# Kernel tuning notes

Measured on AMD Instinct MI355X. Metric: run time of the kernel, lower is better.

Reference implementation:

```python
import jax, jax.numpy as jnp
import numpy as np


def setup_inputs() -> dict:
    key = jax.random.key(0)
    ks = jax.random.split(key, 7)
    B, Nc, Nt = 4, 2048, 2048
    D = 512          # key_size == representation_size
    H, E = 8, 64     # num_heads, head_dim = D // H
    return {
        "keys": jax.random.normal(ks[0], (B, Nc, D), dtype=jnp.float32),
        "values": jax.random.normal(ks[1], (B, Nc, D), dtype=jnp.float32),
        "query": jax.random.normal(ks[2], (B, Nt, D), dtype=jnp.float32),
        "Wk": jax.random.normal(ks[3], (H, D, E), dtype=jnp.float32) * 0.02,
        "Wv": jax.random.normal(ks[4], (H, D, E), dtype=jnp.float32) * 0.02,
        "Wq": jax.random.normal(ks[5], (H, D, E), dtype=jnp.float32) * 0.02,
        "Wout": jax.random.normal(ks[6], (D, D), dtype=jnp.float32) * 0.02,
    }


def reference(keys, values, query, Wk, Wv, Wq, Wout):
    # Batched per-head projections (replaces the per-head Python loop)
    k = jnp.einsum("bnd,hde->bhne", keys, Wk)    # [B,H,Nc,E]
    v = jnp.einsum("bnd,hde->bhne", values, Wv)  # [B,H,Nc,E]
    q = jnp.einsum("bnd,hde->bhne", query, Wq)   # [B,H,Nt,E]
    head_dim = q.shape[-1]
    # NOTE: original scales by head_dim (query.size()[2]), not sqrt(head_dim)
    scores = jnp.einsum("bhqe,bhke->bhqk", q, k) / head_dim
    attn = jax.nn.softmax(scores, axis=-1)
    out = jnp.einsum("bhqk,bhke->bhqe", attn, v)  # [B,H,Nt,E]
    # concat over heads (head-major feature order, matches torch.cat(dim=-1))
    B, H, Nt, E = out.shape
    out = jnp.transpose(out, (0, 2, 1, 3)).reshape(B, Nt, H * E)
    # final Linear (no bias): x @ Wout^T
    return out @ Wout.T
```

## Files before the change

### kernel.cpp

```cpp
#include <hip/hip_runtime.h>

#define B_   4
#define H_   8
#define NSEQ 2048
#define D_   512
#define E_   64

typedef __bf16 bf16x8 __attribute__((ext_vector_type(8)));
typedef float  f32x4  __attribute__((ext_vector_type(4)));

__device__ __forceinline__ unsigned short f2b(float f) {
    __bf16 h = (__bf16)f;
    return __builtin_bit_cast(unsigned short, h);
}
__device__ __forceinline__ bf16x8 ld_frag(const unsigned short* p) {
    return *reinterpret_cast<const bf16x8*>(p);
}
__device__ __forceinline__ void wave_lds_fence() {
    __asm__ __volatile__("s_waitcnt lgkmcnt(0)" ::: "memory");
}
__device__ __forceinline__ void async_copy16(const void* g, const unsigned short* l) {
    __builtin_amdgcn_global_load_lds(
        (const __attribute__((address_space(1))) unsigned int*)g,
        (__attribute__((address_space(3))) unsigned int*)l, 16, 0, 0);
}

__global__ __launch_bounds__(256)
void cast_w_kernel(const float* __restrict__ Wk, const float* __restrict__ Wv,
                   const float* __restrict__ Wq, const float* __restrict__ Wo,
                   unsigned short* __restrict__ okt, unsigned short* __restrict__ ovt,
                   unsigned short* __restrict__ oqt, unsigned short* __restrict__ oo) {
    int idx = blockIdx.x * 256 + threadIdx.x;
    int y = blockIdx.y;
    if (y == 3) { oo[idx] = f2b(Wo[idx]); return; }
    const float* src = y == 0 ? Wk : (y == 1 ? Wv : Wq);
    unsigned short* dst = y == 0 ? okt : (y == 1 ? ovt : oqt);
    float scl = (y == 2) ? 0.015625f : 1.0f;
    int hh = idx >> 15, rem = idx & 32767, d = rem >> 6, e = rem & 63;
    dst[hh * 32768 + e * 512 + d] = f2b(src[idx] * scl);
}

__global__ __launch_bounds__(256)
void xcast_kernel(const float* __restrict__ q, const float* __restrict__ k,
                  const float* __restrict__ v,
                  unsigned short* __restrict__ qx, unsigned short* __restrict__ kx,
                  unsigned short* __restrict__ vx) {
    const int y = blockIdx.y;
    const float* src = y == 0 ? q : (y == 1 ? k : v);
    unsigned short* dst = y == 0 ? qx : (y == 1 ? kx : vx);
    #pragma unroll
    for (int i = 0; i < 4; ++i) {
        int e = blockIdx.x * 4096 + i * 1024 + threadIdx.x * 4;
        float4 f = *reinterpret_cast<const float4*>(src + e);
        *reinterpret_cast<ushort4*>(dst + e) =
            make_ushort4(f2b(f.x), f2b(f.y), f2b(f.z), f2b(f.w));
    }
}

__global__ __launch_bounds__(256, 3)
void proj_gemm(const unsigned short* __restrict__ qx,
               const unsigned short* __restrict__ kx,
               const unsigned short* __restrict__ vx,
               const unsigned short* __restrict__ wqt,
               const unsigned short* __restrict__ wkt,
               const unsigned short* __restrict__ wvt,
               unsigned short* __restrict__ qb, unsigned short* __restrict__ kb,
               unsigned short* __restrict__ vtb) {
    const int m0  = blockIdx.x * 128;
    const int no0 = blockIdx.y * 64;
    const int which = blockIdx.z;
    const int tid = threadIdx.x;
    const int wave = tid >> 6, lane = tid & 63;
    const int quad = lane >> 4, l16 = lane & 15;

    const unsigned short* X = which == 0 ? qx : (which == 1 ? kx : vx);
    const unsigned short* W = which == 0 ? wqt : (which == 1 ? wkt : wvt);

    __shared__ unsigned short Ab[2][8192];
    __shared__ unsigned short Bb[2][4096];

    const unsigned short* Xp = X + (size_t)m0 * D_;
    const unsigned short* Wp = W + (size_t)no0 * D_;

    const int swzF = (l16 & 7) << 4;
    const int r8   = lane >> 3;
    const int sg   = lane & 7;
    const int colK = (sg * 16) ^ ((r8 & 7) << 4);

    #define PROJ_STAGE(kt, buf)                                                \
        {   _Pragma("unroll")                                                  \
            for (int i = 0; i < 4; ++i)                                        \
                async_copy16(                                                  \
                    (const char*)(Xp + (size_t)(wave * 32 + i * 8 + r8) * D_ + \
                                  (kt) * 64) + colK,                           \
                    &Ab[buf][(wave * 32 + i * 8) * 64]);                       \
            _Pragma("unroll")                                                  \
            for (int i = 0; i < 2; ++i)                                        \
                async_copy16(                                                  \
                    (const char*)(Wp + (size_t)(wave * 16 + i * 8 + r8) * D_ + \
                                  (kt) * 64) + colK,                           \
                    &Bb[buf][(wave * 16 + i * 8) * 64]);                       \
        }

    PROJ_STAGE(0, 0)
    __syncthreads();

    const f32x4 z = {0.f, 0.f, 0.f, 0.f};
    f32x4 acc[2][4];
    #pragma unroll
    for (int i = 0; i < 2; ++i)
        #pragma unroll
        for (int j = 0; j < 4; ++j) acc[i][j] = z;

    for (int kt = 0; kt < 8; ++kt) {
        const int cur = kt & 1;
        if (kt + 1 < 8) PROJ_STAGE(kt + 1, 1 - cur)
        #pragma unroll
        for (int kk = 0; kk < 2; ++kk) {
            const int co = ((kk * 64 + quad * 16) ^ swzF) >> 1;
            bf16x8 bfr[4];
            #pragma unroll
            for (int nt = 0; nt < 4; ++nt)
                bfr[nt] = ld_frag(&Bb[cur][(nt * 16 + l16) * 64 + co]);
            #pragma unroll
            for (int mt = 0; mt < 2; ++mt) {
                bf16x8 af = ld_frag(&Ab[cur][(wave * 32 + mt * 16 + l16) * 64 + co]);
                #pragma unroll
                for (int nt = 0; nt < 4; ++nt)
                    acc[mt][nt] = __builtin_amdgcn_mfma_f32_16x16x32_bf16(
                        af, bfr[nt], acc[mt][nt], 0, 0, 0);
            }
        }
        __syncthreads();
    }

    if (which != 2) {
        unsigned short (*Os)[72] = reinterpret_cast<unsigned short(*)[72]>(&Ab[0][0]);
        #pragma unroll
        for (int mt = 0; mt < 2; ++mt)
            #pragma unroll
            for (int nt = 0; nt < 4; ++nt)
                #pragma unroll
                for (int r = 0; r < 4; ++r)
                    Os[wave * 32 + mt * 16 + quad * 4 + r][nt * 16 + l16] =
                        f2b(acc[mt][nt][r]);
        __syncthreads();
        unsigned short* Y = (which == 0 ? qb : kb);
        #pragma unroll
        for (int i = 0; i < 4; ++i) {
            int idx = tid + i * 256;
            int row = idx >> 3, seg = idx & 7;
            *reinterpret_cast<uint4*>(Y + (size_t)(m0 + row) * D_ + no0 + seg * 8) =
                *reinterpret_cast<const uint4*>(&Os[row][seg * 8]);
        }
    } else {
        unsigned short (*Ot)[136] = reinterpret_cast<unsigned short(*)[136]>(&Ab[0][0]);
        #pragma unroll
        for (int mt = 0; mt < 2; ++mt)
            #pragma unroll
            for (int nt = 0; nt < 4; ++nt) {
                ushort4 o = make_ushort4(f2b(acc[mt][nt][0]), f2b(acc[mt][nt][1]),
                                         f2b(acc[mt][nt][2]), f2b(acc[mt][nt][3]));
                *reinterpret_cast<ushort4*>(
                    &Ot[nt * 16 + l16][wave * 32 + mt * 16 + quad * 4]) = o;
            }
        __syncthreads();
        const int b = m0 >> 11, nloc = m0 & 2047;
        #pragma unroll
        for (int i = 0; i < 4; ++i) {
            int idx = tid + i * 256;
            int lhe = idx >> 4, seg = idx & 15;
            int ghe = no0 + lhe;
            *reinterpret_cast<uint4*>(
                vtb + ((size_t)(b * H_ + (ghe >> 6)) * E_ + (ghe & 63)) * NSEQ +
                nloc + seg * 8) =
                *reinterpret_cast<const uint4*>(&Ot[lhe][seg * 8]);
        }
    }
    #undef PROJ_STAGE
}

__global__ __launch_bounds__(256, 4)
void attn_kernel(const unsigned short* __restrict__ qbp,
                 const unsigned short* __restrict__ kbp,
                 const unsigned short* __restrict__ vtbp,
                 unsigned short* __restrict__ aob) {
    const int L = blockIdx.x;
    const int bh = L & 31, qt = L >> 5;
    const int b = bh >> 3, h = bh & 7;
    const int n0 = qt * 64;
    const int tid = threadIdx.x;
    const int wave = tid >> 6, lane = tid & 63;
    const int quad = lane >> 4, l16 = lane & 15;

    __shared__ unsigned short Ks[2][4096];
    __shared__ unsigned short Vs[2][4096];
    __shared__ unsigned short Ps[4096];

    const unsigned short* kbase = kbp + (size_t)(b * NSEQ) * D_ + h * 64;
    const unsigned short* vbase = vtbp + (size_t)(b * H_ + h) * E_ * NSEQ;

    const int swzF = (l16 & 7) << 4;
    const int r8   = lane >> 3;
    const int sg   = lane & 7;
    const int colK = (sg * 16) ^ ((r8 & 7) << 4);

    bf16x8 qf[2];
    #pragma unroll
    for (int kk = 0; kk < 2; ++kk)
        qf[kk] = ld_frag(
            qbp + (size_t)(b * NSEQ + n0 + wave * 16 + l16) * D_ +
            h * 64 + kk * 32 + quad * 8);

    #define ATTN_STAGE(j, buf)                                                 \
        {   _Pragma("unroll")                                                  \
            for (int i = 0; i < 2; ++i) {                                      \
                async_copy16(                                                  \
                    (const char*)(kbase +                                      \
                        (size_t)((j) * 64 + wave * 16 + i * 8 + r8) * D_) + colK, \
                    &Ks[buf][wave * 1024 + i * 512]);                          \
                async_copy16(                                                  \
                    (const char*)(vbase +                                      \
                        (size_t)(wave * 16 + i * 8 + r8) * NSEQ + (j) * 64) + colK, \
                    &Vs[buf][wave * 1024 + i * 512]);                          \
            } }

    ATTN_STAGE(0, 0)
    __syncthreads();

    const f32x4 z = {0.f, 0.f, 0.f, 0.f};
    f32x4 oacc[4] = {z, z, z, z};
    float lacc = 0.f;

    for (int j = 0; j < NSEQ / 64; ++j) {
        const int cur = j & 1;
        if (j + 1 < NSEQ / 64) ATTN_STAGE(j + 1, 1 - cur)

        f32x4 sacc[4] = {z, z, z, z};
        #pragma unroll
        for (int kk = 0; kk < 2; ++kk)
            #pragma unroll
            for (int mg = 0; mg < 4; ++mg) {
                bf16x8 af = ld_frag(&Ks[cur][(mg * 16 + l16) * 64 +
                                             ((((kk * 64 + quad * 16) ^ swzF)) >> 1)]);
                sacc[mg] = __builtin_amdgcn_mfma_f32_16x16x32_bf16(
                    af, qf[kk], sacc[mg], 0, 0, 0);
            }

        {
            float ls = 0.f;
            #pragma unroll
            for (int mg = 0; mg < 4; ++mg) {
                float p0 = __expf(sacc[mg][0]);
                float p1 = __expf(sacc[mg][1]);
                float p2 = __expf(sacc[mg][2]);
                float p3 = __expf(sacc[mg][3]);
                ls += (p0 + p1) + (p2 + p3);
                ushort4 pk = make_ushort4(f2b(p0), f2b(p1), f2b(p2), f2b(p3));
                *reinterpret_cast<ushort4*>(
                    &Ps[(wave * 16 + l16) * 64 +
                        ((((mg * 32 + quad * 8) ^ swzF)) >> 1)]) = pk;
            }
            lacc += ls;
        }
        wave_lds_fence();

        #pragma unroll
        for (int kkv = 0; kkv < 2; ++kkv) {
            bf16x8 pf = ld_frag(&Ps[(wave * 16 + l16) * 64 +
                                    ((((kkv * 64 + quad * 16) ^ swzF)) >> 1)]);
            #pragma unroll
            for (int eg = 0; eg < 4; ++eg) {
                bf16x8 af = ld_frag(&Vs[cur][(eg * 16 + l16) * 64 +
                                             ((((kkv * 64 + quad * 16) ^ swzF)) >> 1)]);
                oacc[eg] = __builtin_amdgcn_mfma_f32_16x16x32_bf16(
                    af, pf, oacc[eg], 0, 0, 0);
            }
        }

        __syncthreads();
    }

    {
        float s = lacc;
        s += __shfl_xor(s, 16);
        s += __shfl_xor(s, 32);
        float li = 1.0f / s;
        unsigned short* op =
            aob + (size_t)(b * NSEQ + n0 + wave * 16 + l16) * D_ + h * 64 + quad * 4;
        #pragma unroll
        for (int eg = 0; eg < 4; ++eg) {
            ushort4 o = make_ushort4(f2b(oacc[eg][0] * li), f2b(oacc[eg][1] * li),
                                     f2b(oacc[eg][2] * li), f2b(oacc[eg][3] * li));
            *reinterpret_cast<ushort4*>(op + eg * 16) = o;
        }
    }
    #undef ATTN_STAGE
}

__global__ __launch_bounds__(256, 3)
void out_gemm(const unsigned short* __restrict__ A,
              const unsigned short* __restrict__ Wo,
              float* __restrict__ Out) {
    const int m0  = blockIdx.x * 128;
    const int no0 = blockIdx.y * 64;
    const int tid = threadIdx.x;
    const int wave = tid >> 6, lane = tid & 63;
    const int quad = lane >> 4, l16 = lane & 15;

    __shared__ unsigned short Ab[2][8192];
    __shared__ unsigned short Bb[2][4096];

    const unsigned short* Ap = A + (size_t)m0 * D_;
    const unsigned short* Bp = Wo + (size_t)no0 * D_;

    const int swzF = (l16 & 7) << 4;
    const int r8   = lane >> 3;
    const int sg   = lane & 7;
    const int colK = (sg * 16) ^ ((r8 & 7) << 4);

    #define OUT_STAGE(kt, buf)                                                 \
        {   _Pragma("unroll")                                                  \
            for (int i = 0; i < 4; ++i)                                        \
                async_copy16(                                                  \
                    (const char*)(Ap + (size_t)(wave * 32 + i * 8 + r8) * D_ + \
                                  (kt) * 64) + colK,                           \
                    &Ab[buf][(wave * 32 + i * 8) * 64]);                       \
            _Pragma("unroll")                                                  \
            for (int i = 0; i < 2; ++i)                                        \
                async_copy16(                                                  \
                    (const char*)(Bp + (size_t)(wave * 16 + i * 8 + r8) * D_ + \
                                  (kt) * 64) + colK,                           \
                    &Bb[buf][(wave * 16 + i * 8) * 64]);                       \
        }

    OUT_STAGE(0, 0)
    __syncthreads();

    const f32x4 z = {0.f, 0.f, 0.f, 0.f};
    f32x4 acc[2][4];
    #pragma unroll
    for (int i = 0; i < 2; ++i)
        #pragma unroll
        for (int j = 0; j < 4; ++j) acc[i][j] = z;

    for (int kt = 0; kt < 8; ++kt) {
        const int cur = kt & 1;
        if (kt + 1 < 8) OUT_STAGE(kt + 1, 1 - cur)
        #pragma unroll
        for (int kk = 0; kk < 2; ++kk) {
            const int co = ((kk * 64 + quad * 16) ^ swzF) >> 1;
            bf16x8 bfr[4];
            #pragma unroll
            for (int nt = 0; nt < 4; ++nt)
                bfr[nt] = ld_frag(&Bb[cur][(nt * 16 + l16) * 64 + co]);
            #pragma unroll
            for (int mt = 0; mt < 2; ++mt) {
                bf16x8 af = ld_frag(&Ab[cur][(wave * 32 + mt * 16 + l16) * 64 + co]);
                #pragma unroll
                for (int nt = 0; nt < 4; ++nt)
                    acc[mt][nt] = __builtin_amdgcn_mfma_f32_16x16x32_bf16(
                        af, bfr[nt], acc[mt][nt], 0, 0, 0);
            }
        }
        __syncthreads();
    }
    #pragma unroll
    for (int mt = 0; mt < 2; ++mt)
        #pragma unroll
        for (int nt = 0; nt < 4; ++nt)
            #pragma unroll
            for (int r = 0; r < 4; ++r)
                Out[(size_t)(m0 + wave * 32 + mt * 16 + quad * 4 + r) * D_ +
                    no0 + nt * 16 + l16] = acc[mt][nt][r];
    #undef OUT_STAGE
}

extern "C" void kernel_launch(void* const* d_in, const int* in_sizes, int n_in,
                              void* d_out, int out_size, void* d_ws, size_t ws_size,
                              hipStream_t stream) {
    const float* keys   = (const float*)d_in[0];
    const float* values = (const float*)d_in[1];
    const float* query  = (const float*)d_in[2];
    const float* Wk     = (const float*)d_in[3];
    const float* Wv     = (const float*)d_in[4];
    const float* Wq     = (const float*)d_in[5];
    const float* Wout   = (const float*)d_in[6];
    float* out = (float*)d_out;

    unsigned short* ws16 = (unsigned short*)d_ws;
    const size_t XN = (size_t)B_ * NSEQ * D_;
    const size_t WN = (size_t)H_ * D_ * E_;
    unsigned short* wkt = ws16;
    unsigned short* wvt = wkt + WN;
    unsigned short* wqt = wvt + WN;
    unsigned short* wob = wqt + WN;
    unsigned short* qb  = wob + WN;
    unsigned short* kb  = qb + XN;
    unsigned short* vtb = kb + XN;
    unsigned short* aob = vtb + XN;
    unsigned short* qx  = aob + XN;
    unsigned short* kx  = qx + XN;
    unsigned short* vx  = aob;

    cast_w_kernel<<<dim3(1024, 4), 256, 0, stream>>>(Wk, Wv, Wq, Wout,
                                                     wkt, wvt, wqt, wob);

    xcast_kernel<<<dim3(1024, 3), 256, 0, stream>>>(query, keys, values,
                                                    qx, kx, vx);

    proj_gemm<<<dim3(64, 8, 3), 256, 0, stream>>>(
        qx, kx, vx, wqt, wkt, wvt, qb, kb, vtb);

    attn_kernel<<<dim3(1024), 256, 0, stream>>>(qb, kb, vtb, aob);

    out_gemm<<<dim3(64, 8), 256, 0, stream>>>(aob, wob, out);
}
```

Before: 190.3 us.

## Use two waves per attention block, each handling 32 query rows

The attention kernel now runs 128 threads (2 waves) per block instead of 4 waves. Each wave processes two 16-row query groups, so every K and V fragment read from LDS feeds two MFMAs. This halves LDS fragment traffic per MFMA. The cost is more accumulator registers per wave, fewer waves per block to hide latency, and more async-copy work per thread.

```diff
diff --git a/kernel.cpp b/kernel.cpp
--- a/kernel.cpp
+++ b/kernel.cpp
@@ -180,7 +180,7 @@
     #undef PROJ_STAGE
 }
 
-__global__ __launch_bounds__(256, 4)
+__global__ __launch_bounds__(128, 2)
 void attn_kernel(const unsigned short* __restrict__ qbp,
                  const unsigned short* __restrict__ kbp,
                  const unsigned short* __restrict__ vtbp,
@@ -205,93 +205,113 @@
     const int sg   = lane & 7;
     const int colK = (sg * 16) ^ ((r8 & 7) << 4);
 
-    bf16x8 qf[2];
-    #pragma unroll
-    for (int kk = 0; kk < 2; ++kk)
-        qf[kk] = ld_frag(
-            qbp + (size_t)(b * NSEQ + n0 + wave * 16 + l16) * D_ +
-            h * 64 + kk * 32 + quad * 8);
+    bf16x8 qf[2][2];
+    #pragma unroll
+    for (int qg = 0; qg < 2; ++qg)
+        #pragma unroll
+        for (int kk = 0; kk < 2; ++kk)
+            qf[qg][kk] = ld_frag(
+                qbp + (size_t)(b * NSEQ + n0 + wave * 32 + qg * 16 + l16) * D_ +
+                h * 64 + kk * 32 + quad * 8);
 
     #define ATTN_STAGE(j, buf)                                                 \
         {   _Pragma("unroll")                                                  \
-            for (int i = 0; i < 2; ++i) {                                      \
+            for (int i = 0; i < 4; ++i) {                                      \
                 async_copy16(                                                  \
                     (const char*)(kbase +                                      \
-                        (size_t)((j) * 64 + wave * 16 + i * 8 + r8) * D_) + colK, \
-                    &Ks[buf][wave * 1024 + i * 512]);                          \
+                        (size_t)((j) * 64 + wave * 32 + i * 8 + r8) * D_) + colK, \
+                    &Ks[buf][(wave * 32 + i * 8) * 64]);                       \
                 async_copy16(                                                  \
                     (const char*)(vbase +                                      \
-                        (size_t)(wave * 16 + i * 8 + r8) * NSEQ + (j) * 64) + colK, \
-                    &Vs[buf][wave * 1024 + i * 512]);                          \
+                        (size_t)(wave * 32 + i * 8 + r8) * NSEQ + (j) * 64) + colK, \
+                    &Vs[buf][(wave * 32 + i * 8) * 64]);                       \
             } }
 
     ATTN_STAGE(0, 0)
     __syncthreads();
 
     const f32x4 z = {0.f, 0.f, 0.f, 0.f};
-    f32x4 oacc[4] = {z, z, z, z};
-    float lacc = 0.f;
+    f32x4 oacc[2][4];
+    #pragma unroll
+    for (int qg = 0; qg < 2; ++qg)
+        #pragma unroll
+        for (int eg = 0; eg < 4; ++eg) oacc[qg][eg] = z;
+    float lacc[2] = {0.f, 0.f};
 
     for (int j = 0; j < NSEQ / 64; ++j) {
         const int cur = j & 1;
         if (j + 1 < NSEQ / 64) ATTN_STAGE(j + 1, 1 - cur)
 
-        f32x4 sacc[4] = {z, z, z, z};
-        #pragma unroll
-        for (int kk = 0; kk < 2; ++kk)
+        f32x4 sacc[2][4];
+        #pragma unroll
+        for (int qg = 0; qg < 2; ++qg)
+            #pragma unroll
+            for (int mg = 0; mg < 4; ++mg) sacc[qg][mg] = z;
+        #pragma unroll
+        for (int kk = 0; kk < 2; ++kk) {
+            const int co = ((kk * 64 + quad * 16) ^ swzF) >> 1;
             #pragma unroll
             for (int mg = 0; mg < 4; ++mg) {
-                bf16x8 af = ld_frag(&Ks[cur][(mg * 16 + l16) * 64 +
-                                             ((((kk * 64 + quad * 16) ^ swzF)) >> 1)]);
-                sacc[mg] = __builtin_amdgcn_mfma_f32_16x16x32_bf16(
-                    af, qf[kk], sacc[mg], 0, 0, 0);
-            }
-
-        {
+                bf16x8 af = ld_frag(&Ks[cur][(mg * 16 + l16) * 64 + co]);
+                sacc[0][mg] = __builtin_amdgcn_mfma_f32_16x16x32_bf16(
+                    af, qf[0][kk], sacc[0][mg], 0, 0, 0);
+                sacc[1][mg] = __builtin_amdgcn_mfma_f32_16x16x32_bf16(
+                    af, qf[1][kk], sacc[1][mg], 0, 0, 0);
+            }
+        }
+
+        #pragma unroll
+        for (int qg = 0; qg < 2; ++qg) {
             float ls = 0.f;
+            const int prow = (wave * 32 + qg * 16 + l16) * 64;
             #pragma unroll
             for (int mg = 0; mg < 4; ++mg) {
-                float p0 = __expf(sacc[mg][0]);
-                float p1 = __expf(sacc[mg][1]);
-                float p2 = __expf(sacc[mg][2]);
-                float p3 = __expf(sacc[mg][3]);
+                float p0 = __expf(sacc[qg][mg][0]);
+                float p1 = __expf(sacc[qg][mg][1]);
+                float p2 = __expf(sacc[qg][mg][2]);
+                float p3 = __expf(sacc[qg][mg][3]);
                 ls += (p0 + p1) + (p2 + p3);
                 ushort4 pk = make_ushort4(f2b(p0), f2b(p1), f2b(p2), f2b(p3));
                 *reinterpret_cast<ushort4*>(
-                    &Ps[(wave * 16 + l16) * 64 +
-                        ((((mg * 32 + quad * 8) ^ swzF)) >> 1)]) = pk;
-            }
-            lacc += ls;
+                    &Ps[prow + ((((mg * 32 + quad * 8) ^ swzF)) >> 1)]) = pk;
+            }
+            lacc[qg] += ls;
         }
         wave_lds_fence();
 
         #pragma unroll
         for (int kkv = 0; kkv < 2; ++kkv) {
-            bf16x8 pf = ld_frag(&Ps[(wave * 16 + l16) * 64 +
-                                    ((((kkv * 64 + quad * 16) ^ swzF)) >> 1)]);
+            const int co = ((kkv * 64 + quad * 16) ^ swzF) >> 1;
+            bf16x8 pf0 = ld_frag(&Ps[(wave * 32 + l16) * 64 + co]);
+            bf16x8 pf1 = ld_frag(&Ps[(wave * 32 + 16 + l16) * 64 + co]);
             #pragma unroll
             for (int eg = 0; eg < 4; ++eg) {
-                bf16x8 af = ld_frag(&Vs[cur][(eg * 16 + l16) * 64 +
-                                             ((((kkv * 64 + quad * 16) ^ swzF)) >> 1)]);
-                oacc[eg] = __builtin_amdgcn_mfma_f32_16x16x32_bf16(
-                    af, pf, oacc[eg], 0, 0, 0);
+                bf16x8 af = ld_frag(&Vs[cur][(eg * 16 + l16) * 64 + co]);
+                oacc[0][eg] = __builtin_amdgcn_mfma_f32_16x16x32_bf16(
+                    af, pf0, oacc[0][eg], 0, 0, 0);
+                oacc[1][eg] = __builtin_amdgcn_mfma_f32_16x16x32_bf16(
+                    af, pf1, oacc[1][eg], 0, 0, 0);
             }
         }
 
         __syncthreads();
     }
 
-    {
-        float s = lacc;
+    #pragma unroll
+    for (int qg = 0; qg < 2; ++qg) {
+        float s = lacc[qg];
         s += __shfl_xor(s, 16);
         s += __shfl_xor(s, 32);
         float li = 1.0f / s;
         unsigned short* op =
-            aob + (size_t)(b * NSEQ + n0 + wave * 16 + l16) * D_ + h * 64 + quad * 4;
+            aob + (size_t)(b * NSEQ + n0 + wave * 32 + qg * 16 + l16) * D_ +
+            h * 64 + quad * 4;
         #pragma unroll
         for (int eg = 0; eg < 4; ++eg) {
-            ushort4 o = make_ushort4(f2b(oacc[eg][0] * li), f2b(oacc[eg][1] * li),
-                                     f2b(oacc[eg][2] * li), f2b(oacc[eg][3] * li));
+            ushort4 o = make_ushort4(f2b(oacc[qg][eg][0] * li),
+                                     f2b(oacc[qg][eg][1] * li),
+                                     f2b(oacc[qg][eg][2] * li),
+                                     f2b(oacc[qg][eg][3] * li));
             *reinterpret_cast<ushort4*>(op + eg * 16) = o;
         }
     }
@@ -412,7 +432,7 @@
     proj_gemm<<<dim3(64, 8, 3), 256, 0, stream>>>(
         qx, kx, vx, wqt, wkt, wvt, qb, kb, vtb);
 
-    attn_kernel<<<dim3(1024), 256, 0, stream>>>(qb, kb, vtb, aob);
+    attn_kernel<<<dim3(1024), 128, 0, stream>>>(qb, kb, vtb, aob);
 
     out_gemm<<<dim3(64, 8), 256, 0, stream>>>(aob, wob, out);
 }
```

Measured after the change: 196.1 us. 3.1% more time.

## Use 32x32 MFMA in attention with register-resident P and split-K waves

Applied to the files above, without the earlier changes.

Restructures the attention kernel to use 32x32x16 bf16 MFMA tiles. Each wave computes a 32-query by 32-key score block, and waves are split across the key halves. The probability tile is kept in registers via v_permlane32_swap instead of being staged through LDS, which removes the Ps buffer and its store/fence/reload. Partial outputs from the two key-half waves are reduced through LDS at the end. This adds an epilogue reduction, more accumulator registers and lower occupancy (launch bounds 4→3).

```diff
diff --git a/kernel.cpp b/kernel.cpp
--- a/kernel.cpp
+++ b/kernel.cpp
@@ -8,16 +8,17 @@
 
 typedef __bf16 bf16x8 __attribute__((ext_vector_type(8)));
 typedef float  f32x4  __attribute__((ext_vector_type(4)));
+typedef float  f32x16 __attribute__((ext_vector_type(16)));
 
 __device__ __forceinline__ unsigned short f2b(float f) {
     __bf16 h = (__bf16)f;
     return __builtin_bit_cast(unsigned short, h);
 }
+__device__ __forceinline__ unsigned pk2(float a, float b) {
+    return (unsigned)f2b(a) | ((unsigned)f2b(b) << 16);
+}
 __device__ __forceinline__ bf16x8 ld_frag(const unsigned short* p) {
     return *reinterpret_cast<const bf16x8*>(p);
-}
-__device__ __forceinline__ void wave_lds_fence() {
-    __asm__ __volatile__("s_waitcnt lgkmcnt(0)" ::: "memory");
 }
 __device__ __forceinline__ void async_copy16(const void* g, const unsigned short* l) {
     __builtin_amdgcn_global_load_lds(
@@ -180,7 +181,7 @@
     #undef PROJ_STAGE
 }
 
-__global__ __launch_bounds__(256, 4)
+__global__ __launch_bounds__(256, 3)
 void attn_kernel(const unsigned short* __restrict__ qbp,
                  const unsigned short* __restrict__ kbp,
                  const unsigned short* __restrict__ vtbp,
@@ -191,26 +192,25 @@
     const int n0 = qt * 64;
     const int tid = threadIdx.x;
     const int wave = tid >> 6, lane = tid & 63;
-    const int quad = lane >> 4, l16 = lane & 15;
+    const int wk = wave >> 1, wq = wave & 1;
+    const int l32 = lane & 31, hi = lane >> 5;
 
     __shared__ unsigned short Ks[2][4096];
     __shared__ unsigned short Vs[2][4096];
-    __shared__ unsigned short Ps[4096];
 
     const unsigned short* kbase = kbp + (size_t)(b * NSEQ) * D_ + h * 64;
     const unsigned short* vbase = vtbp + (size_t)(b * H_ + h) * E_ * NSEQ;
 
-    const int swzF = (l16 & 7) << 4;
     const int r8   = lane >> 3;
     const int sg   = lane & 7;
     const int colK = (sg * 16) ^ ((r8 & 7) << 4);
-
-    bf16x8 qf[2];
+    const int swz  = (lane & 7) << 4;
+
+    bf16x8 qf[4];
     #pragma unroll
-    for (int kk = 0; kk < 2; ++kk)
-        qf[kk] = ld_frag(
-            qbp + (size_t)(b * NSEQ + n0 + wave * 16 + l16) * D_ +
-            h * 64 + kk * 32 + quad * 8);
+    for (int ks = 0; ks < 4; ++ks)
+        qf[ks] = ld_frag(qbp + (size_t)(b * NSEQ + n0 + wq * 32 + l32) * D_ +
+                         h * 64 + ks * 16 + hi * 8);
 
     #define ATTN_STAGE(j, buf)                                                 \
         {   _Pragma("unroll")                                                  \
@@ -228,72 +228,85 @@
     ATTN_STAGE(0, 0)
     __syncthreads();
 
-    const f32x4 z = {0.f, 0.f, 0.f, 0.f};
-    f32x4 oacc[4] = {z, z, z, z};
+    f32x16 oacc[2] = {};
     float lacc = 0.f;
 
     for (int j = 0; j < NSEQ / 64; ++j) {
         const int cur = j & 1;
         if (j + 1 < NSEQ / 64) ATTN_STAGE(j + 1, 1 - cur)
 
-        f32x4 sacc[4] = {z, z, z, z};
-        #pragma unroll
-        for (int kk = 0; kk < 2; ++kk)
-            #pragma unroll
-            for (int mg = 0; mg < 4; ++mg) {
-                bf16x8 af = ld_frag(&Ks[cur][(mg * 16 + l16) * 64 +
-                                             ((((kk * 64 + quad * 16) ^ swzF)) >> 1)]);
-                sacc[mg] = __builtin_amdgcn_mfma_f32_16x16x32_bf16(
-                    af, qf[kk], sacc[mg], 0, 0, 0);
-            }
-
-        {
-            float ls = 0.f;
-            #pragma unroll
-            for (int mg = 0; mg < 4; ++mg) {
-                float p0 = __expf(sacc[mg][0]);
-                float p1 = __expf(sacc[mg][1]);
-                float p2 = __expf(sacc[mg][2]);
-                float p3 = __expf(sacc[mg][3]);
-                ls += (p0 + p1) + (p2 + p3);
-                ushort4 pk = make_ushort4(f2b(p0), f2b(p1), f2b(p2), f2b(p3));
-                *reinterpret_cast<ushort4*>(
-                    &Ps[(wave * 16 + l16) * 64 +
-                        ((((mg * 32 + quad * 8) ^ swzF)) >> 1)]) = pk;
-            }
-            lacc += ls;
-        }
-        wave_lds_fence();
-
-        #pragma unroll
-        for (int kkv = 0; kkv < 2; ++kkv) {
-            bf16x8 pf = ld_frag(&Ps[(wave * 16 + l16) * 64 +
-                                    ((((kkv * 64 + quad * 16) ^ swzF)) >> 1)]);
-            #pragma unroll
-            for (int eg = 0; eg < 4; ++eg) {
-                bf16x8 af = ld_frag(&Vs[cur][(eg * 16 + l16) * 64 +
-                                             ((((kkv * 64 + quad * 16) ^ swzF)) >> 1)]);
-                oacc[eg] = __builtin_amdgcn_mfma_f32_16x16x32_bf16(
-                    af, pf, oacc[eg], 0, 0, 0);
+        const unsigned short* Kc = Ks[cur];
+        const unsigned short* Vc = Vs[cur];
+
+        f32x16 sacc = {};
+        #pragma unroll
+        for (int ks = 0; ks < 4; ++ks) {
+            bf16x8 kf = ld_frag(
+                &Kc[(wk * 32 + l32) * 64 + ((((ks * 32 + hi * 16)) ^ swz) >> 1)]);
+            sacc = __builtin_amdgcn_mfma_f32_32x32x16_bf16(kf, qf[ks], sacc, 0, 0, 0);
+        }
+
+        float p[16];
+        #pragma unroll
+        for (int r = 0; r < 16; ++r) p[r] = __expf(sacc[r]);
+        lacc += ((p[0] + p[1]) + (p[2] + p[3])) + ((p[4] + p[5]) + (p[6] + p[7])) +
+                (((p[8] + p[9]) + (p[10] + p[11])) + ((p[12] + p[13]) + (p[14] + p[15])));
+
+        #pragma unroll
+        for (int s = 0; s < 2; ++s) {
+            unsigned x0 = pk2(p[s * 8 + 0], p[s * 8 + 1]);
+            unsigned x1 = pk2(p[s * 8 + 2], p[s * 8 + 3]);
+            unsigned y0 = pk2(p[s * 8 + 4], p[s * 8 + 5]);
+            unsigned y1 = pk2(p[s * 8 + 6], p[s * 8 + 7]);
+            asm volatile("v_permlane32_swap_b32 %0, %1" : "+v"(x0), "+v"(y0));
+            asm volatile("v_permlane32_swap_b32 %0, %1" : "+v"(x1), "+v"(y1));
+            uint4 u = make_uint4(x0, x1, y0, y1);
+            bf16x8 pb = __builtin_bit_cast(bf16x8, u);
+            #pragma unroll
+            for (int eb = 0; eb < 2; ++eb) {
+                bf16x8 vf = ld_frag(
+                    &Vc[(eb * 32 + l32) * 64 +
+                        ((((wk * 64 + s * 32 + hi * 16)) ^ swz) >> 1)]);
+                oacc[eb] = __builtin_amdgcn_mfma_f32_32x32x16_bf16(
+                    vf, pb, oacc[eb], 0, 0, 0);
             }
         }
 
         __syncthreads();
     }
 
-    {
-        float s = lacc;
-        s += __shfl_xor(s, 16);
-        s += __shfl_xor(s, 32);
-        float li = 1.0f / s;
+    lacc += __shfl_xor(lacc, 32);
+    float* Of = reinterpret_cast<float*>(&Ks[0][0]);
+    float* Lf = reinterpret_cast<float*>(&Vs[0][0]);
+    if (wk == 0) {
+        #pragma unroll
+        for (int eb = 0; eb < 2; ++eb)
+            #pragma unroll
+            for (int rg = 0; rg < 4; ++rg) {
+                f32x4 v = {oacc[eb][rg * 4 + 0], oacc[eb][rg * 4 + 1],
+                           oacc[eb][rg * 4 + 2], oacc[eb][rg * 4 + 3]};
+                *reinterpret_cast<f32x4*>(
+                    &Of[(wq * 32 + l32) * 64 + eb * 32 + rg * 8 + hi * 4]) = v;
+            }
+        if (hi == 0) Lf[wq * 32 + l32] = lacc;
+    }
+    __syncthreads();
+    if (wk == 1) {
+        const float li = 1.0f / (lacc + Lf[wq * 32 + l32]);
         unsigned short* op =
-            aob + (size_t)(b * NSEQ + n0 + wave * 16 + l16) * D_ + h * 64 + quad * 4;
-        #pragma unroll
-        for (int eg = 0; eg < 4; ++eg) {
-            ushort4 o = make_ushort4(f2b(oacc[eg][0] * li), f2b(oacc[eg][1] * li),
-                                     f2b(oacc[eg][2] * li), f2b(oacc[eg][3] * li));
-            *reinterpret_cast<ushort4*>(op + eg * 16) = o;
-        }
+            aob + (size_t)(b * NSEQ + n0 + wq * 32 + l32) * D_ + h * 64;
+        #pragma unroll
+        for (int eb = 0; eb < 2; ++eb)
+            #pragma unroll
+            for (int rg = 0; rg < 4; ++rg) {
+                const f32x4 o = *reinterpret_cast<const f32x4*>(
+                    &Of[(wq * 32 + l32) * 64 + eb * 32 + rg * 8 + hi * 4]);
+                ushort4 st = make_ushort4(f2b((oacc[eb][rg * 4 + 0] + o.x) * li),
+                                          f2b((oacc[eb][rg * 4 + 1] + o.y) * li),
+                                          f2b((oacc[eb][rg * 4 + 2] + o.z) * li),
+                                          f2b((oacc[eb][rg * 4 + 3] + o.w) * li));
+                *reinterpret_cast<ushort4*>(op + eb * 32 + rg * 8 + hi * 4) = st;
+            }
     }
     #undef ATTN_STAGE
 }
```

Result: no change. 187.2 us (-1.6%).
